# Performance work log

Measured on AMD Instinct MI355X. Metric: run time of the kernel, lower is better.

The kernel has to match this reference:

```python
import jax, jax.numpy as jnp
import numpy as np

B, S, D, N, NC = 2, 1024, 1024, 8192, 8


def _srw_chunked(x, h, emb_norm, tau_offset, w_read, w_write, n_chunks):
    Bd, Sd, Dd = x.shape
    Nd = emb_norm.shape[0]
    cs = Nd // n_chunks
    h_bf = h.astype(jnp.bfloat16)
    x_bf = x.astype(jnp.bfloat16)
    emb_bf = emb_norm.astype(jnp.bfloat16)
    read_bf = w_read.astype(jnp.bfloat16)
    write_bf = w_write.astype(jnp.bfloat16)
    z1 = jnp.zeros((Bd, Sd, 1))

    @jax.checkpoint
    def estimate_stats(h, emb, nc_val):
        ec0 = jax.lax.dynamic_slice_in_dim(emb, 0, cs, axis=0)
        sc0 = h @ ec0.T
        s_sum = sc0.sum(axis=-1, keepdims=True).astype(jnp.float32) * nc_val
        sq_sum = (sc0 ** 2).sum(axis=-1, keepdims=True).astype(jnp.float32) * nc_val
        return (s_sum, sq_sum)

    s_sum, sq_sum = estimate_stats(h_bf, emb_bf, n_chunks)
    s_mean = s_sum / Nd
    s_std = jnp.sqrt(sq_sum / Nd - s_mean ** 2) + 1e-08
    tau = s_mean + tau_offset * s_std
    tau_bf = tau.astype(jnp.bfloat16)

    @jax.checkpoint
    def gsrw_step(carry, i):
        out, es, em, ac, lbs, lbq = carry
        s = i * cs
        ec = jax.lax.dynamic_slice_in_dim(emb_bf, s, cs, axis=0)
        rc = jax.lax.dynamic_slice_in_dim(read_bf, s, cs, axis=0)
        wc = jax.lax.dynamic_slice_in_dim(write_bf, s, cs, axis=0)
        sc = h_bf @ ec.T  # [B,S,cs]
        raw = sc - tau_bf
        gc = jnp.where(raw > 0, raw, (1e-06 * jnp.exp(jnp.clip(raw.astype(jnp.float32), -10.0, 0.0))).astype(jnp.bfloat16))
        gc = jnp.clip(gc, 0.0, 10.0)
        eg = (jnp.exp(gc.astype(jnp.float32)) - 1.0).astype(jnp.bfloat16)
        ef = eg.astype(jnp.float32)
        xr = x_bf @ rc.T  # [B,S,cs]
        co = ((eg * xr) @ wc).astype(jnp.float32)  # [B,S,D]
        gn = ef.mean(axis=(0, 1))
        lbs = lbs + gn.sum()
        lbq = lbq + (gn ** 2).sum()
        return ((out + co,
                 es + ef.sum(axis=-1, keepdims=True),
                 jnp.maximum(em, ef.max(axis=-1, keepdims=True)),
                 ac + (raw > 0).sum(axis=-1, keepdims=True).astype(jnp.float32),
                 lbs, lbq), None)

    z_scalar = jnp.float32(0.0)
    init = (jnp.zeros((Bd, Sd, Dd), dtype=jnp.float32), z1,
            jnp.full((Bd, Sd, 1), -1000000000.0), z1, z_scalar, z_scalar)
    (raw_out, tes, tem, tac, lb_sum, lb_sq), _ = jax.lax.scan(gsrw_step, init, jnp.arange(n_chunks))
    inv_es = (1.0 / (tes + 1e-08)).astype(jnp.bfloat16)
    gs = jnp.tanh(tem).astype(jnp.bfloat16)
    out = raw_out * inv_es * gs
    exp_sum_scalar = tes.mean() + 1e-08
    norm_lb_sum = lb_sum / exp_sum_scalar
    norm_lb_sq = lb_sq / exp_sum_scalar ** 2
    lb_loss = norm_lb_sq * Nd - 2.0 * norm_lb_sum + 1.0
    gs_mean = jnp.tanh(tem).mean()
    es_mean = tes.mean()
    return (out.astype(jnp.float32), tac / Nd, tem, lb_loss, gs_mean, es_mean)


def setup_inputs() -> dict:
    key = jax.random.key(0)
    k = jax.random.split(key, 6)
    x = jax.random.normal(k[0], (B, S, D), jnp.float32)
    h = jax.random.normal(k[1], (B, S, D), jnp.float32)
    emb = jax.random.normal(k[2], (N, D), jnp.float32) * 0.02
    w_read = jax.random.normal(k[3], (N, D), jnp.float32) * 0.02
    w_write = jax.random.normal(k[4], (N, D), jnp.float32) * 0.02
    tau_offset = jax.random.normal(k[5], (B, S, 1), jnp.float32) * 0.1
    return {"x": x, "h": h, "emb": emb, "tau_offset": tau_offset,
            "w_read": w_read, "w_write": w_write, "n_chunks": NC}


def reference(x, h, emb, tau_offset, w_read, w_write, n_chunks):
    # caller (_know_forward) unit-normalizes the embedding pool first
    emb_norm = emb / (jnp.linalg.norm(emb, axis=-1, keepdims=True) + 1e-08)
    out, active_frac, gate_max, lb_loss, gs_mean, es_mean = _srw_chunked(
        x, h, emb_norm, tau_offset, w_read, w_write, n_chunks)
    return out
```

## Files before the change

kernel.cpp:

```cpp
#include <hip/hip_runtime.h>


#define MDIM 2048
#define DDIM 1024
#define NDIM 8192

typedef __attribute__((ext_vector_type(8))) __bf16 bf16x8;
typedef __attribute__((ext_vector_type(4))) float f32x4;

static __device__ __forceinline__ unsigned short f2b(float f) {
  unsigned u = __float_as_uint(f);
  u = (u + 0x7FFFu + ((u >> 16) & 1u)) >> 16;
  return (unsigned short)u;
}
static __device__ __forceinline__ float b2f(unsigned short s) {
  return __uint_as_float(((unsigned)s) << 16);
}

#define LDSF(off) (*(const bf16x8*)(lds + (off)))
#define MFMA_BF16 __builtin_amdgcn_mfma_f32_16x16x32_bf16

#define GLOAD_LDS(gp, lp)                                                              \
  __builtin_amdgcn_global_load_lds(                                                    \
      (const __attribute__((address_space(1))) unsigned int*)(const void*)(gp),        \
      (__attribute__((address_space(3))) unsigned int*)(void*)(lp), 16, 0, 0)

static __device__ __forceinline__ void stage_half(const unsigned short* __restrict__ src,
                                                  int ld, int row0, int k0,
                                                  char* lds, int lds_off, int w, int l) {
  const int rsub = l >> 3;
  const int col = k0 + 8 * ((l & 7) ^ rsub);
#pragma unroll
  for (int j = 0; j < 2; ++j) {
    const unsigned short* g =
        src + (size_t)(row0 + w * 8 + j * 64 + rsub) * (size_t)ld + col;
    GLOAD_LDS(g, lds + lds_off + j * 8192 + w * 1024);
  }
}

static __device__ __forceinline__ void stage4(const unsigned short* __restrict__ asrc,
                                              const unsigned short* __restrict__ bsrc,
                                              int ld, int m0, int n0, int k0,
                                              char* lds, int buf, int w, int l) {
  stage_half(asrc, ld, m0,       k0, lds, buf,         w, l);
  stage_half(asrc, ld, m0 + 128, k0, lds, buf + 16384, w, l);
  stage_half(bsrc, ld, n0,       k0, lds, buf + 32768, w, l);
  stage_half(bsrc, ld, n0 + 128, k0, lds, buf + 49152, w, l);
}

static __device__ __forceinline__ void gemm256(const unsigned short* __restrict__ asrc,
                                               const unsigned short* __restrict__ bsrc,
                                               int ld, int m0, int n0, int kbase,
                                               char* lds, f32x4 (&acc)[8][4],
                                               int w, int l, int wr, int wc) {
  const int lrow = l & 15, lk = l >> 4;
  const int axor = (l & 7) << 4;
  const int kx0 = (lk << 4) ^ axor;
  const int kx1 = (64 | (lk << 4)) ^ axor;
  const int arow_off = lrow * 128;
  const int brow_off = ((wc & 1) * 64 + lrow) * 128;

  stage4(asrc, bsrc, ld, m0, n0, kbase, lds, 0, w, l);
  asm volatile("s_waitcnt vmcnt(0)" ::: "memory");
  __builtin_amdgcn_s_barrier();

#pragma unroll 1
  for (int t = 0; t < 16; ++t) {
    const int buf = (t & 1) * 65536;
    const int nbuf = 65536 - buf;
    if (t < 15) stage4(asrc, bsrc, ld, m0, n0, kbase + (t + 1) * 64, lds, nbuf, w, l);

    const int ab = buf + wr * 16384;
    const int bb = buf + 32768 + (wc >> 1) * 16384;
    bf16x8 aLO[4][2], aHI[4][2], bLO[2][2], bHI[2][2];
#pragma unroll
    for (int m = 0; m < 4; ++m) {
      aLO[m][0] = LDSF(ab + arow_off + m * 2048 + kx0);
      aLO[m][1] = LDSF(ab + arow_off + m * 2048 + kx1);
    }
#pragma unroll
    for (int n = 0; n < 2; ++n) {
      bLO[n][0] = LDSF(bb + brow_off + n * 2048 + kx0);
      bLO[n][1] = LDSF(bb + brow_off + n * 2048 + kx1);
      bHI[n][0] = LDSF(bb + brow_off + (n + 2) * 2048 + kx0);
      bHI[n][1] = LDSF(bb + brow_off + (n + 2) * 2048 + kx1);
    }
    asm volatile("s_waitcnt lgkmcnt(0)" ::: "memory");
    __builtin_amdgcn_s_setprio(1);
#pragma unroll
    for (int ks = 0; ks < 2; ++ks)
#pragma unroll
      for (int n = 0; n < 2; ++n)
#pragma unroll
        for (int m = 0; m < 4; ++m)
          acc[m][n] = MFMA_BF16(aLO[m][ks], bLO[n][ks], acc[m][n], 0, 0, 0);
    __builtin_amdgcn_s_setprio(0);
#pragma unroll
    for (int m = 0; m < 4; ++m) {
      aHI[m][0] = LDSF(ab + arow_off + (m + 4) * 2048 + kx0);
      aHI[m][1] = LDSF(ab + arow_off + (m + 4) * 2048 + kx1);
    }
    __builtin_amdgcn_s_setprio(1);
#pragma unroll
    for (int ks = 0; ks < 2; ++ks)
#pragma unroll
      for (int n = 0; n < 2; ++n)
#pragma unroll
        for (int m = 0; m < 4; ++m)
          acc[m][n + 2] = MFMA_BF16(aLO[m][ks], bHI[n][ks], acc[m][n + 2], 0, 0, 0);
    __builtin_amdgcn_s_setprio(0);
    asm volatile("s_waitcnt lgkmcnt(0)" ::: "memory");
    __builtin_amdgcn_s_setprio(1);
#pragma unroll
    for (int ks = 0; ks < 2; ++ks)
#pragma unroll
      for (int n = 0; n < 2; ++n)
#pragma unroll
        for (int m = 0; m < 4; ++m)
          acc[m + 4][n + 2] = MFMA_BF16(aHI[m][ks], bHI[n][ks], acc[m + 4][n + 2], 0, 0, 0);
#pragma unroll
    for (int ks = 0; ks < 2; ++ks)
#pragma unroll
      for (int n = 0; n < 2; ++n)
#pragma unroll
        for (int m = 0; m < 4; ++m)
          acc[m + 4][n] = MFMA_BF16(aHI[m][ks], bLO[n][ks], acc[m + 4][n], 0, 0, 0);
    __builtin_amdgcn_s_setprio(0);
    asm volatile("s_waitcnt vmcnt(0)" ::: "memory");
    __builtin_amdgcn_s_barrier();
  }
}


__global__ __launch_bounds__(256) void k_prep(const float* __restrict__ emb,
                                              const float* __restrict__ w_read,
                                              const float* __restrict__ h,
                                              const float* __restrict__ x,
                                              const float* __restrict__ w_write,
                                              unsigned short* __restrict__ eb,
                                              unsigned short* __restrict__ rb,
                                              unsigned short* __restrict__ hb,
                                              unsigned short* __restrict__ xb,
                                              unsigned short* __restrict__ wbT) {
  const int b = blockIdx.x, t = threadIdx.x;
  if (b < 2048) {
    __shared__ float tsm[64][65];
    const int nb = b & 127, db = b >> 7;
    const int r = t >> 2, c4 = (t & 3) * 16;
#pragma unroll
    for (int j = 0; j < 4; ++j) {
      const float4 v = *(const float4*)&w_write[(size_t)(nb * 64 + r) * 1024 + db * 64 + c4 + 4 * j];
      tsm[r][c4 + 4 * j + 0] = v.x;
      tsm[r][c4 + 4 * j + 1] = v.y;
      tsm[r][c4 + 4 * j + 2] = v.z;
      tsm[r][c4 + 4 * j + 3] = v.w;
    }
    __syncthreads();
    const int dr = t >> 2, nc0 = (t & 3) * 16;
    unsigned pk[8];
#pragma unroll
    for (int j = 0; j < 8; ++j) {
      const unsigned lo = f2b(tsm[nc0 + 2 * j][dr]);
      const unsigned hi = f2b(tsm[nc0 + 2 * j + 1][dr]);
      pk[j] = lo | (hi << 16);
    }
    uint4* dst = (uint4*)(wbT + (size_t)(db * 64 + dr) * 8192 + nb * 64 + nc0);
    uint4 w0, w1;
    w0.x = pk[0]; w0.y = pk[1]; w0.z = pk[2]; w0.w = pk[3];
    w1.x = pk[4]; w1.y = pk[5]; w1.z = pk[6]; w1.w = pk[7];
    dst[0] = w0;
    dst[1] = w1;
  } else if (b < 10240) {
    const int n = b - 2048;
    const float4 v = ((const float4*)(emb + (size_t)n * 1024))[t];
    float ss = v.x * v.x + v.y * v.y + v.z * v.z + v.w * v.w;
#pragma unroll
    for (int off = 1; off < 64; off <<= 1) ss += __shfl_xor(ss, off, 64);
    __shared__ float wsum[4];
    if ((t & 63) == 0) wsum[t >> 6] = ss;
    __syncthreads();
    const float denom = sqrtf(wsum[0] + wsum[1] + wsum[2] + wsum[3]) + 1e-8f;
    ushort4 o;
    o.x = f2b(v.x / denom);
    o.y = f2b(v.y / denom);
    o.z = f2b(v.z / denom);
    o.w = f2b(v.w / denom);
    ((ushort4*)(eb + (size_t)n * 1024))[t] = o;
  } else {
    const float* src;
    unsigned short* dst;
    int i;
    if (b < 18432) { src = w_read; dst = rb; i = (b - 10240) * 256 + t; }
    else if (b < 20480) { src = h; dst = hb; i = (b - 18432) * 256 + t; }
    else { src = x; dst = xb; i = (b - 20480) * 256 + t; }
    const float4 v = ((const float4*)src)[i];
    ushort4 o;
    o.x = f2b(v.x);
    o.y = f2b(v.y);
    o.z = f2b(v.z);
    o.w = f2b(v.w);
    ((ushort4*)dst)[i] = o;
  }
}


template <int TROWS>
static __device__ __forceinline__ void stage_tile(const unsigned short* __restrict__ src,
                                                  int row0, int k0, int ld,
                                                  unsigned short* lds, int wave, int lane) {
  const int rsub = lane >> 3;
  const int csub = (lane & 7) << 3;
#pragma unroll
  for (int q = 0; q < TROWS / 32; ++q) {
    const int p = q * 4 + wave;
    const unsigned short* g =
        src + (size_t)(row0 + p * 8 + rsub) * (size_t)ld + (size_t)(k0 + csub);
    GLOAD_LDS(g, lds + p * 512);
  }
}

__global__ __launch_bounds__(256, 2) void k_stats(const unsigned short* __restrict__ hb,
                                                  const unsigned short* __restrict__ eb,
                                                  float* __restrict__ stat_s,
                                                  float* __restrict__ stat_q) {
  __shared__ unsigned short a_sm[64 * 64];
  __shared__ unsigned short b_sm[128 * 64];
  __shared__ float red_s[2][64];
  __shared__ float red_q[2][64];
  const int t = threadIdx.x;
  const int wave = t >> 6, lane = t & 63;
  const int wr = wave >> 1, wc = wave & 1;
  const int m0 = blockIdx.x * 64, n0 = blockIdx.y * 128;
  const int arow = lane & 15;
  const int kcol = (lane >> 4) << 3;
  f32x4 acc[2][4];
#pragma unroll
  for (int m = 0; m < 2; ++m)
#pragma unroll
    for (int n = 0; n < 4; ++n) acc[m][n] = (f32x4)0.0f;
  for (int k0 = 0; k0 < 1024; k0 += 64) {
    stage_tile<64>(hb, m0, k0, 1024, a_sm, wave, lane);
    stage_tile<128>(eb, n0, k0, 1024, b_sm, wave, lane);
    asm volatile("s_waitcnt vmcnt(0)" ::: "memory");
    __syncthreads();
#pragma unroll
    for (int ks = 0; ks < 2; ++ks) {
      bf16x8 af[2], bfr[4];
#pragma unroll
      for (int m = 0; m < 2; ++m)
        af[m] = *(const bf16x8*)&a_sm[(wr * 32 + m * 16 + arow) * 64 + ks * 32 + kcol];
#pragma unroll
      for (int n = 0; n < 4; ++n)
        bfr[n] = *(const bf16x8*)&b_sm[(wc * 64 + n * 16 + arow) * 64 + ks * 32 + kcol];
#pragma unroll
      for (int m = 0; m < 2; ++m)
#pragma unroll
        for (int n = 0; n < 4; ++n)
          acc[m][n] = MFMA_BF16(af[m], bfr[n], acc[m][n], 0, 0, 0);
    }
    __syncthreads();
  }

  float s_r[2][4], q_r[2][4];
#pragma unroll
  for (int m = 0; m < 2; ++m)
#pragma unroll
    for (int i = 0; i < 4; ++i) { s_r[m][i] = 0.f; q_r[m][i] = 0.f; }
#pragma unroll
  for (int m = 0; m < 2; ++m)
#pragma unroll
    for (int n = 0; n < 4; ++n)
#pragma unroll
      for (int i = 0; i < 4; ++i) {
        const float scf = b2f(f2b(acc[m][n][i]));
        s_r[m][i] += scf;
        q_r[m][i] += b2f(f2b(scf * scf));
      }
#pragma unroll
  for (int m = 0; m < 2; ++m)
#pragma unroll
    for (int i = 0; i < 4; ++i) {
      float s = s_r[m][i], q = q_r[m][i];
      for (int off = 1; off < 16; off <<= 1) {
        s += __shfl_xor(s, off, 64);
        q += __shfl_xor(q, off, 64);
      }
      if ((lane & 15) == 0) {
        const int rloc = wr * 32 + m * 16 + (lane >> 4) * 4 + i;
        red_s[wc][rloc] = s;
        red_q[wc][rloc] = q;
      }
    }
  __syncthreads();
  if (t < 64) {
    stat_s[(size_t)(m0 + t) * 8 + blockIdx.y] = red_s[0][t] + red_s[1][t];
    stat_q[(size_t)(m0 + t) * 8 + blockIdx.y] = red_q[0][t] + red_q[1][t];
  }
}


__global__ __launch_bounds__(512, 2) void k_sc(const unsigned short* __restrict__ hb,
                                               const unsigned short* __restrict__ eb,
                                               const float* __restrict__ stat_s,
                                               const float* __restrict__ stat_q,
                                               const float* __restrict__ tau_off,
                                               unsigned short* __restrict__ Aeg,
                                               float* __restrict__ es_part,
                                               float* __restrict__ em_part) {
  __shared__ __align__(16) char lds[131072];
  const int t = threadIdx.x, w = t >> 6, l = t & 63;
  const int wr = w >> 2, wc = w & 3;
  const int bid = blockIdx.x;
  const int swz = (bid & 7) * 32 + (bid >> 3);
  const int m0 = (swz >> 5) * 256, n0 = (swz & 31) * 256;
  f32x4 acc[8][4];
#pragma unroll
  for (int m = 0; m < 8; ++m)
#pragma unroll
    for (int n = 0; n < 4; ++n) acc[m][n] = (f32x4)0.0f;
  gemm256(hb, eb, 1024, m0, n0, 0, lds, acc, w, l, wr, wc);

  __syncthreads();
  float* tau_sm = (float*)lds;
  float* red_es = (float*)(lds + 1024);
  float* red_em = (float*)(lds + 1024 + 4096);
  if (t < 256) {
    const int r = m0 + t;
    float S = 0.f, Q = 0.f;
#pragma unroll
    for (int j = 0; j < 8; ++j) {
      S += stat_s[(size_t)r * 8 + j];
      Q += stat_q[(size_t)r * 8 + j];
    }
    const float s_sum = S * 8.0f;
    const float sq_sum = Q * 8.0f;
    const float mean = s_sum * (1.0f / 8192.0f);
    const float var = __fsub_rn(sq_sum * (1.0f / 8192.0f), __fmul_rn(mean, mean));
    const float sd = __fadd_rn(__fsqrt_rn(var), 1e-8f);
    const float tv = __fadd_rn(mean, __fmul_rn(tau_off[r], sd));
    tau_sm[t] = b2f(f2b(tv));
  }
  __syncthreads();
  const int lrow = l & 15, lk = l >> 4;
#pragma unroll
  for (int m = 0; m < 8; ++m) {
#pragma unroll
    for (int i = 0; i < 4; ++i) {
      const int rl = wr * 128 + m * 16 + lk * 4 + i;
      const float taub = tau_sm[rl];
      float es_v = 0.f, em_v = 0.f;
#pragma unroll
      for (int n = 0; n < 4; ++n) {
        const float scf = b2f(f2b(acc[m][n][i]));
        const float rawf = b2f(f2b(scf - taub));
        float gcf;
        if (rawf > 0.f) gcf = fminf(rawf, 10.0f);
        else gcf = b2f(f2b(1e-6f * expf(fmaxf(rawf, -10.0f))));
        const unsigned short egu = f2b(expf(gcf) - 1.0f);
        const float ef = b2f(egu);
        es_v += ef;
        em_v = fmaxf(em_v, ef);
        Aeg[(size_t)(m0 + rl) * NDIM + (size_t)(n0 + wc * 64 + n * 16 + lrow)] = egu;
      }
      for (int off = 1; off < 16; off <<= 1) {
        es_v += __shfl_xor(es_v, off, 64);
        em_v = fmaxf(em_v, __shfl_xor(em_v, off, 64));
      }
      if (lrow == 0) {
        red_es[wc * 256 + rl] = es_v;
        red_em[wc * 256 + rl] = em_v;
      }
    }
  }
  __syncthreads();
  if (t < 256) {
    const float s = red_es[t] + red_es[256 + t] + red_es[512 + t] + red_es[768 + t];
    const float e = fmaxf(fmaxf(red_em[t], red_em[256 + t]),
                          fmaxf(red_em[512 + t], red_em[768 + t]));
    es_part[(size_t)(m0 + t) * 32 + (n0 >> 8)] = s;
    em_part[(size_t)(m0 + t) * 32 + (n0 >> 8)] = e;
  }
}


__global__ __launch_bounds__(512, 2) void k_xr(const unsigned short* __restrict__ xb,
                                               const unsigned short* __restrict__ rb,
                                               unsigned short* __restrict__ Aeg) {
  __shared__ __align__(16) char lds[131072];
  const int t = threadIdx.x, w = t >> 6, l = t & 63;
  const int wr = w >> 2, wc = w & 3;
  const int bid = blockIdx.x;
  const int swz = (bid & 7) * 32 + (bid >> 3);
  const int m0 = (swz >> 5) * 256, n0 = (swz & 31) * 256;
  f32x4 acc[8][4];
#pragma unroll
  for (int m = 0; m < 8; ++m)
#pragma unroll
    for (int n = 0; n < 4; ++n) acc[m][n] = (f32x4)0.0f;
  gemm256(xb, rb, 1024, m0, n0, 0, lds, acc, w, l, wr, wc);

  const int lrow = l & 15, lk = l >> 4;
#pragma unroll
  for (int m = 0; m < 8; ++m)
#pragma unroll
    for (int n = 0; n < 4; ++n)
#pragma unroll
      for (int i = 0; i < 4; ++i) {
        const int rl = wr * 128 + m * 16 + lk * 4 + i;
        const size_t idx =
            (size_t)(m0 + rl) * NDIM + (size_t)(n0 + wc * 64 + n * 16 + lrow);
        const unsigned short egu = Aeg[idx];
        const float xrf = b2f(f2b(acc[m][n][i]));
        Aeg[idx] = f2b(b2f(egu) * xrf);
      }
}


__global__ __launch_bounds__(512, 2) void k_out(const unsigned short* __restrict__ A,
                                                const unsigned short* __restrict__ wbT,
                                                unsigned short* __restrict__ pacc) {
  __shared__ __align__(16) char lds[131072];
  const int t = threadIdx.x, w = t >> 6, l = t & 63;
  const int wr = w >> 2, wc = w & 3;
  const int bid = blockIdx.x;
  const int swz = (bid & 7) * 32 + (bid >> 3);
  const int bm = swz >> 5, chunk = (swz >> 2) & 7, bd = swz & 3;
  const int m0 = bm * 256, d0 = bd * 256;
  f32x4 acc[8][4];
#pragma unroll
  for (int m = 0; m < 8; ++m)
#pragma unroll
    for (int n = 0; n < 4; ++n) acc[m][n] = (f32x4)0.0f;
  gemm256(A, wbT, 8192, m0, d0, chunk * 1024, lds, acc, w, l, wr, wc);

  const int lrow = l & 15, lk = l >> 4;
#pragma unroll
  for (int m = 0; m < 8; ++m)
#pragma unroll
    for (int n = 0; n < 4; ++n)
#pragma unroll
      for (int i = 0; i < 4; ++i) {
        const int rl = wr * 128 + m * 16 + lk * 4 + i;
        pacc[((size_t)chunk * MDIM + (m0 + rl)) * DDIM +
             (size_t)(d0 + wc * 64 + n * 16 + lrow)] = f2b(acc[m][n][i]);
      }
}


__global__ __launch_bounds__(256) void k_finish(const unsigned short* __restrict__ pacc,
                                                const float* __restrict__ es_part,
                                                const float* __restrict__ em_part,
                                                float* __restrict__ outp) {
  const int t = blockIdx.x * 256 + threadIdx.x;
  const int r = t >> 8;
  const int d4 = (t & 255) * 4;
  float s = 0.f, m = 0.f;
#pragma unroll
  for (int j = 0; j < 32; ++j) {
    s += es_part[(size_t)r * 32 + j];
    m = fmaxf(m, em_part[(size_t)r * 32 + j]);
  }
  const float inv = b2f(f2b(1.0f / (s + 1e-8f)));
  const float gsv = b2f(f2b(tanhf(m)));
  float sx = 0.f, sy = 0.f, sz = 0.f, sw = 0.f;
#pragma unroll
  for (int c = 0; c < 8; ++c) {
    const ushort4 v = *(const ushort4*)(pacc + ((size_t)c * MDIM + r) * DDIM + d4);
    sx += b2f(v.x);
    sy += b2f(v.y);
    sz += b2f(v.z);
    sw += b2f(v.w);
  }
  float4 o;
  o.x = (sx * inv) * gsv;
  o.y = (sy * inv) * gsv;
  o.z = (sz * inv) * gsv;
  o.w = (sw * inv) * gsv;
  *(float4*)(outp + (size_t)r * DDIM + d4) = o;
}


extern "C" void kernel_launch(void* const* d_in, const int* in_sizes, int n_in,
                              void* d_out, int out_size, void* d_ws, size_t ws_size,
                              hipStream_t stream) {
  const float* x = (const float*)d_in[0];
  const float* h = (const float*)d_in[1];
  const float* emb = (const float*)d_in[2];
  const float* tau_off = (const float*)d_in[3];
  const float* w_read = (const float*)d_in[4];
  const float* w_write = (const float*)d_in[5];

  char* ws = (char*)d_ws;
  const size_t MB = 1024 * 1024;
  unsigned short* rb = (unsigned short*)(ws);
  unsigned short* eb = (unsigned short*)(ws + 16 * MB);
  unsigned short* wbT = (unsigned short*)(ws + 32 * MB);
  unsigned short* hb = (unsigned short*)(ws + 48 * MB);
  unsigned short* xb = (unsigned short*)(ws + 52 * MB);
  unsigned short* Aeg = (unsigned short*)(ws + 56 * MB);
  unsigned short* pacc = (unsigned short*)(ws);
  float* stat_s = (float*)(ws + 88 * MB + 1 * 65536);
  float* stat_q = (float*)(ws + 88 * MB + 2 * 65536);
  float* es_part = (float*)(ws + 88 * MB + 3 * 65536);
  float* em_part = (float*)(ws + 88 * MB + 7 * 65536);
  if (ws_size < 88 * MB + 11 * 65536) return;
  float* outp = (float*)d_out;

  k_prep<<<22528, 256, 0, stream>>>(emb, w_read, h, x, w_write, eb, rb, hb, xb, wbT);
  k_stats<<<dim3(MDIM / 64, 8), 256, 0, stream>>>(hb, eb, stat_s, stat_q);
  k_sc<<<256, 512, 0, stream>>>(hb, eb, stat_s, stat_q, tau_off, Aeg, es_part, em_part);
  k_xr<<<256, 512, 0, stream>>>(xb, rb, Aeg);
  k_out<<<256, 512, 0, stream>>>(Aeg, wbT, pacc);
  k_finish<<<(MDIM * DDIM / 4) / 256, 256, 0, stream>>>(pacc, es_part, em_part, outp);
}
```

Measured before the change: 186.7 us.

## Split GEMM K-tile into staged quarter loads with finer waitcnt pipelining

Restructures the shared 256x256 GEMM main loop so that global-to-LDS staging of the next tile is split into four half-tile loads, each issued between MFMA phases. Partial vmcnt waits and an extra mid-tile barrier replace the single full wait per iteration. The warp-to-tile mapping is also changed to an interleaved row/column layout, and the epilogue indices are updated to match. The aim is to overlap memory latency with compute and reduce stalls at barriers, at the cost of more barriers and tighter correctness constraints on the LDS buffer reuse.

```diff
diff --git a/kernel.cpp b/kernel.cpp
--- a/kernel.cpp
+++ b/kernel.cpp
@@ -38,14 +38,89 @@
   }
 }
 
-static __device__ __forceinline__ void stage4(const unsigned short* __restrict__ asrc,
+template <int PAR, bool STG, int VM1, int VM3>
+static __device__ __forceinline__ void ktile4(const unsigned short* __restrict__ asrc,
                                               const unsigned short* __restrict__ bsrc,
-                                              int ld, int m0, int n0, int k0,
-                                              char* lds, int buf, int w, int l) {
-  stage_half(asrc, ld, m0,       k0, lds, buf,         w, l);
-  stage_half(asrc, ld, m0 + 128, k0, lds, buf + 16384, w, l);
-  stage_half(bsrc, ld, n0,       k0, lds, buf + 32768, w, l);
-  stage_half(bsrc, ld, n0 + 128, k0, lds, buf + 49152, w, l);
+                                              int ld, int m0, int n0, int kS,
+                                              char* lds, f32x4 (&acc)[8][4],
+                                              int w, int l, int a_off, int b_off,
+                                              int kx0, int kx1) {
+  const int buf = PAR * 65536;
+  const int nbuf = 65536 - buf;
+  bf16x8 aLO[4][2], aHI[4][2], bLO[2][2], bHI[2][2];
+
+  if (STG) stage_half(bsrc, ld, n0, kS, lds, nbuf + 32768, w, l);
+#pragma unroll
+  for (int m = 0; m < 4; ++m) {
+    aLO[m][0] = LDSF(buf + a_off + m * 2048 + kx0);
+    aLO[m][1] = LDSF(buf + a_off + m * 2048 + kx1);
+  }
+#pragma unroll
+  for (int n = 0; n < 2; ++n) {
+    bLO[n][0] = LDSF(buf + 32768 + b_off + n * 2048 + kx0);
+    bLO[n][1] = LDSF(buf + 32768 + b_off + n * 2048 + kx1);
+  }
+  asm volatile("s_waitcnt lgkmcnt(0)" ::: "memory");
+  __builtin_amdgcn_s_setprio(1);
+#pragma unroll
+  for (int ks = 0; ks < 2; ++ks)
+#pragma unroll
+    for (int n = 0; n < 2; ++n)
+#pragma unroll
+      for (int m = 0; m < 4; ++m)
+        acc[m][n] = MFMA_BF16(aLO[m][ks], bLO[n][ks], acc[m][n], 0, 0, 0);
+  __builtin_amdgcn_s_setprio(0);
+
+  if (STG) stage_half(bsrc, ld, n0 + 128, kS, lds, nbuf + 49152, w, l);
+#pragma unroll
+  for (int n = 0; n < 2; ++n) {
+    bHI[n][0] = LDSF(buf + 49152 + b_off + n * 2048 + kx0);
+    bHI[n][1] = LDSF(buf + 49152 + b_off + n * 2048 + kx1);
+  }
+  asm volatile("s_waitcnt lgkmcnt(0)" ::: "memory");
+  __builtin_amdgcn_s_setprio(1);
+#pragma unroll
+  for (int ks = 0; ks < 2; ++ks)
+#pragma unroll
+    for (int n = 0; n < 2; ++n)
+#pragma unroll
+      for (int m = 0; m < 4; ++m)
+        acc[m][n + 2] = MFMA_BF16(aLO[m][ks], bHI[n][ks], acc[m][n + 2], 0, 0, 0);
+  __builtin_amdgcn_s_setprio(0);
+  if (VM1 == 4) asm volatile("s_waitcnt vmcnt(4)" ::: "memory");
+  if (VM1 == 0) asm volatile("s_waitcnt vmcnt(0)" ::: "memory");
+  __builtin_amdgcn_s_barrier();
+
+  if (STG) stage_half(asrc, ld, m0, kS, lds, nbuf, w, l);
+#pragma unroll
+  for (int m = 0; m < 4; ++m) {
+    aHI[m][0] = LDSF(buf + 16384 + a_off + m * 2048 + kx0);
+    aHI[m][1] = LDSF(buf + 16384 + a_off + m * 2048 + kx1);
+  }
+  asm volatile("s_waitcnt lgkmcnt(0)" ::: "memory");
+  __builtin_amdgcn_s_setprio(1);
+#pragma unroll
+  for (int ks = 0; ks < 2; ++ks)
+#pragma unroll
+    for (int n = 0; n < 2; ++n)
+#pragma unroll
+      for (int m = 0; m < 4; ++m)
+        acc[m + 4][n + 2] = MFMA_BF16(aHI[m][ks], bHI[n][ks], acc[m + 4][n + 2], 0, 0, 0);
+  __builtin_amdgcn_s_setprio(0);
+
+  if (STG) stage_half(asrc, ld, m0 + 128, kS, lds, nbuf + 16384, w, l);
+  __builtin_amdgcn_s_setprio(1);
+#pragma unroll
+  for (int ks = 0; ks < 2; ++ks)
+#pragma unroll
+    for (int n = 0; n < 2; ++n)
+#pragma unroll
+      for (int m = 0; m < 4; ++m)
+        acc[m + 4][n] = MFMA_BF16(aHI[m][ks], bLO[n][ks], acc[m + 4][n], 0, 0, 0);
+  __builtin_amdgcn_s_setprio(0);
+  if (VM3 == 2) asm volatile("s_waitcnt vmcnt(2)" ::: "memory");
+  if (VM3 == 0) asm volatile("s_waitcnt vmcnt(0)" ::: "memory");
+  __builtin_amdgcn_s_barrier();
 }
 
 static __device__ __forceinline__ void gemm256(const unsigned short* __restrict__ asrc,
@@ -57,79 +132,31 @@
   const int axor = (l & 7) << 4;
   const int kx0 = (lk << 4) ^ axor;
   const int kx1 = (64 | (lk << 4)) ^ axor;
-  const int arow_off = lrow * 128;
-  const int brow_off = ((wc & 1) * 64 + lrow) * 128;
-
-  stage4(asrc, bsrc, ld, m0, n0, kbase, lds, 0, w, l);
-  asm volatile("s_waitcnt vmcnt(0)" ::: "memory");
+  const int a_off = wr * 8192 + lrow * 128;
+  const int b_off = wc * 4096 + lrow * 128;
+
+  stage_half(bsrc, ld, n0,       kbase, lds, 32768, w, l);
+  stage_half(bsrc, ld, n0 + 128, kbase, lds, 49152, w, l);
+  stage_half(asrc, ld, m0,       kbase, lds, 0,     w, l);
+  stage_half(asrc, ld, m0 + 128, kbase, lds, 16384, w, l);
+  asm volatile("s_waitcnt vmcnt(2)" ::: "memory");
   __builtin_amdgcn_s_barrier();
 
 #pragma unroll 1
-  for (int t = 0; t < 16; ++t) {
-    const int buf = (t & 1) * 65536;
-    const int nbuf = 65536 - buf;
-    if (t < 15) stage4(asrc, bsrc, ld, m0, n0, kbase + (t + 1) * 64, lds, nbuf, w, l);
-
-    const int ab = buf + wr * 16384;
-    const int bb = buf + 32768 + (wc >> 1) * 16384;
-    bf16x8 aLO[4][2], aHI[4][2], bLO[2][2], bHI[2][2];
-#pragma unroll
-    for (int m = 0; m < 4; ++m) {
-      aLO[m][0] = LDSF(ab + arow_off + m * 2048 + kx0);
-      aLO[m][1] = LDSF(ab + arow_off + m * 2048 + kx1);
-    }
-#pragma unroll
-    for (int n = 0; n < 2; ++n) {
-      bLO[n][0] = LDSF(bb + brow_off + n * 2048 + kx0);
-      bLO[n][1] = LDSF(bb + brow_off + n * 2048 + kx1);
-      bHI[n][0] = LDSF(bb + brow_off + (n + 2) * 2048 + kx0);
-      bHI[n][1] = LDSF(bb + brow_off + (n + 2) * 2048 + kx1);
-    }
-    asm volatile("s_waitcnt lgkmcnt(0)" ::: "memory");
-    __builtin_amdgcn_s_setprio(1);
-#pragma unroll
-    for (int ks = 0; ks < 2; ++ks)
-#pragma unroll
-      for (int n = 0; n < 2; ++n)
-#pragma unroll
-        for (int m = 0; m < 4; ++m)
-          acc[m][n] = MFMA_BF16(aLO[m][ks], bLO[n][ks], acc[m][n], 0, 0, 0);
-    __builtin_amdgcn_s_setprio(0);
-#pragma unroll
-    for (int m = 0; m < 4; ++m) {
-      aHI[m][0] = LDSF(ab + arow_off + (m + 4) * 2048 + kx0);
-      aHI[m][1] = LDSF(ab + arow_off + (m + 4) * 2048 + kx1);
-    }
-    __builtin_amdgcn_s_setprio(1);
-#pragma unroll
-    for (int ks = 0; ks < 2; ++ks)
-#pragma unroll
-      for (int n = 0; n < 2; ++n)
-#pragma unroll
-        for (int m = 0; m < 4; ++m)
-          acc[m][n + 2] = MFMA_BF16(aLO[m][ks], bHI[n][ks], acc[m][n + 2], 0, 0, 0);
-    __builtin_amdgcn_s_setprio(0);
-    asm volatile("s_waitcnt lgkmcnt(0)" ::: "memory");
-    __builtin_amdgcn_s_setprio(1);
-#pragma unroll
-    for (int ks = 0; ks < 2; ++ks)
-#pragma unroll
-      for (int n = 0; n < 2; ++n)
-#pragma unroll
-        for (int m = 0; m < 4; ++m)
-          acc[m + 4][n + 2] = MFMA_BF16(aHI[m][ks], bHI[n][ks], acc[m + 4][n + 2], 0, 0, 0);
-#pragma unroll
-    for (int ks = 0; ks < 2; ++ks)
-#pragma unroll
-      for (int n = 0; n < 2; ++n)
-#pragma unroll
-        for (int m = 0; m < 4; ++m)
-          acc[m + 4][n] = MFMA_BF16(aHI[m][ks], bLO[n][ks], acc[m + 4][n], 0, 0, 0);
-    __builtin_amdgcn_s_setprio(0);
-    asm volatile("s_waitcnt vmcnt(0)" ::: "memory");
-    __builtin_amdgcn_s_barrier();
-  }
-}
+  for (int t = 0; t < 14; t += 2) {
+    ktile4<0, true, 4, 2>(asrc, bsrc, ld, m0, n0, kbase + (t + 1) * 64, lds, acc,
+                          w, l, a_off, b_off, kx0, kx1);
+    ktile4<1, true, 4, 2>(asrc, bsrc, ld, m0, n0, kbase + (t + 2) * 64, lds, acc,
+                          w, l, a_off, b_off, kx0, kx1);
+  }
+  ktile4<0, true, 4, 2>(asrc, bsrc, ld, m0, n0, kbase + 15 * 64, lds, acc,
+                        w, l, a_off, b_off, kx0, kx1);
+  ktile4<1, false, 0, -1>(asrc, bsrc, ld, m0, n0, 0, lds, acc,
+                          w, l, a_off, b_off, kx0, kx1);
+}
+
+#define RLIDX(m, i) (((m) >> 2) * 128 + wr * 64 + ((m) & 3) * 16 + lk * 4 + (i))
+#define CLIDX(n) (((n) >> 1) * 128 + wc * 32 + ((n) & 1) * 16 + lrow)
 
 
 __global__ __launch_bounds__(256) void k_prep(const float* __restrict__ emb,
@@ -346,7 +373,7 @@
   for (int m = 0; m < 8; ++m) {
 #pragma unroll
     for (int i = 0; i < 4; ++i) {
-      const int rl = wr * 128 + m * 16 + lk * 4 + i;
+      const int rl = RLIDX(m, i);
       const float taub = tau_sm[rl];
       float es_v = 0.f, em_v = 0.f;
 #pragma unroll
@@ -360,7 +387,7 @@
         const float ef = b2f(egu);
         es_v += ef;
         em_v = fmaxf(em_v, ef);
-        Aeg[(size_t)(m0 + rl) * NDIM + (size_t)(n0 + wc * 64 + n * 16 + lrow)] = egu;
+        Aeg[(size_t)(m0 + rl) * NDIM + (size_t)(n0 + CLIDX(n))] = egu;
       }
       for (int off = 1; off < 16; off <<= 1) {
         es_v += __shfl_xor(es_v, off, 64);
@@ -406,9 +433,8 @@
     for (int n = 0; n < 4; ++n)
 #pragma unroll
       for (int i = 0; i < 4; ++i) {
-        const int rl = wr * 128 + m * 16 + lk * 4 + i;
-        const size_t idx =
-            (size_t)(m0 + rl) * NDIM + (size_t)(n0 + wc * 64 + n * 16 + lrow);
+        const int rl = RLIDX(m, i);
+        const size_t idx = (size_t)(m0 + rl) * NDIM + (size_t)(n0 + CLIDX(n));
         const unsigned short egu = Aeg[idx];
         const float xrf = b2f(f2b(acc[m][n][i]));
         Aeg[idx] = f2b(b2f(egu) * xrf);
@@ -440,9 +466,9 @@
     for (int n = 0; n < 4; ++n)
 #pragma unroll
       for (int i = 0; i < 4; ++i) {
-        const int rl = wr * 128 + m * 16 + lk * 4 + i;
-        pacc[((size_t)chunk * MDIM + (m0 + rl)) * DDIM +
-             (size_t)(d0 + wc * 64 + n * 16 + lrow)] = f2b(acc[m][n][i]);
+        const int rl = RLIDX(m, i);
+        pacc[((size_t)chunk * MDIM + (m0 + rl)) * DDIM + (size_t)(d0 + CLIDX(n))] =
+            f2b(acc[m][n][i]);
       }
 }
 
```

Result: slower. 197.5 us (+5.8%).
